# Optimization experiments

Measured on AMD Instinct MI355X. Metric: run time of the kernel, lower is better.

The kernel has to match this reference:

```python
import jax, jax.numpy as jnp
import numpy as np
import math

HIDDEN = 1024
HEADS = 16
HEAD_DIM = HIDDEN // HEADS


def setup_inputs() -> dict:
    key = jax.random.key(0)
    ks = jax.random.split(key, 7)
    B, S = 2, 2048
    scale = 1.0 / math.sqrt(HIDDEN)
    return {
        "x": jax.random.normal(ks[0], (B, S, HIDDEN), dtype=jnp.float32),
        "Wq": jax.random.normal(ks[1], (HIDDEN, HIDDEN), dtype=jnp.float32) * scale,
        "Wk": jax.random.normal(ks[2], (HIDDEN, HIDDEN), dtype=jnp.float32) * scale,
        "Wv": jax.random.normal(ks[3], (HIDDEN, HIDDEN), dtype=jnp.float32) * scale,
        "Wo": jax.random.normal(ks[4], (HIDDEN, HIDDEN), dtype=jnp.float32) * scale,
        "quantum_phase": jax.random.normal(ks[5], (HEADS, HEAD_DIM), dtype=jnp.float32),
        "quantum_amplitude": jnp.ones((HEADS, HEAD_DIM), dtype=jnp.float32),
    }


def reference(x, Wq, Wk, Wv, Wo, quantum_phase, quantum_amplitude):
    B, S, d = x.shape
    H, D = HEADS, HEAD_DIM

    # per-head/per-channel quantum modulation: real(x*exp(i*phase)) == x*cos(phase)
    mod = (jnp.cos(quantum_phase) * quantum_amplitude)[None, :, None, :]  # [1,H,1,D]

    def proj(W):
        return (x @ W).reshape(B, S, H, D).transpose(0, 2, 1, 3)  # [B,H,S,D]

    q = proj(Wq) * mod
    k = proj(Wk) * mod
    v = proj(Wv) * mod

    scores = jnp.einsum("bhid,bhjd->bhij", q, k) / math.sqrt(D)  # [B,H,S,S]

    # quantum interference: scores[i,j] *= cos(2*pi*(i-j)/S)
    idx = jnp.arange(S, dtype=jnp.float32)
    cos_mat = jnp.cos(2.0 * math.pi * (idx[:, None] - idx[None, :]) / S)  # [S,S]
    scores = scores * cos_mat

    w = jax.nn.softmax(scores, axis=-1)
    # superposition of attention weights with key-rolled copy
    w = (w + jnp.roll(w, 1, axis=-1)) / math.sqrt(2.0)

    out = jnp.einsum("bhij,bhjd->bhid", w, v)  # [B,H,S,D]
    out = out.transpose(0, 2, 1, 3).reshape(B, S, d)
    return out @ Wo
```

## Files before the change

kernel.cpp:

```cpp
#include <hip/hip_runtime.h>
#include <hip/hip_bf16.h>
#include <math.h>

#define HIDDEN 1024
#define HEADS  16
#define HDIM   64
#define BATCH  2
#define SEQ    2048
#define ROWS   (BATCH*SEQ)
#define BH     (BATCH*HEADS)

typedef __attribute__((ext_vector_type(8))) short  short8;
typedef __attribute__((ext_vector_type(8))) __bf16 bf16x8;
typedef __attribute__((ext_vector_type(4))) float  f32x4;

static __device__ __forceinline__ unsigned short f2bf(float f) {
    unsigned int u = __builtin_bit_cast(unsigned int, f);
    u += 0x7FFFu + ((u >> 16) & 1u);
    return (unsigned short)(u >> 16);
}
static __device__ __forceinline__ float bf2f(unsigned short h) {
    unsigned int u = ((unsigned int)h) << 16;
    return __builtin_bit_cast(float, u);
}
static __device__ __forceinline__ f32x4 mfma16(short8 a, short8 b, f32x4 c) {
    return __builtin_amdgcn_mfma_f32_16x16x32_bf16(
        __builtin_bit_cast(bf16x8, a), __builtin_bit_cast(bf16x8, b), c, 0, 0, 0);
}
static __device__ __forceinline__ void gl_lds16(const unsigned short* g, unsigned short* l) {
    __builtin_amdgcn_global_load_lds(
        (const __attribute__((address_space(1))) unsigned int*)g,
        (__attribute__((address_space(3))) unsigned int*)l, 16, 0, 0);
}

__global__ void convert_x_kernel(const float* __restrict__ x, unsigned short* __restrict__ xb,
                                 const float* __restrict__ qp, const float* __restrict__ qa,
                                 float* __restrict__ mod, float* __restrict__ mod2,
                                 float* __restrict__ posc, float* __restrict__ poss) {
    int i = (blockIdx.x * 256 + threadIdx.x) * 4;
    float4 v = *(const float4*)(x + i);
    ushort4 o;
    o.x = f2bf(v.x); o.y = f2bf(v.y); o.z = f2bf(v.z); o.w = f2bf(v.w);
    *(ushort4*)(xb + i) = o;
    if (blockIdx.x < 8) {
        int k = blockIdx.x * 256 + threadIdx.x;
        if (k < HIDDEN) {
            float m = cosf(qp[k]) * qa[k];
            mod[k] = m;
            mod2[k] = m * m * 0.18033688011112042f;
        }
        if (k < SEQ) {
            float ang = (float)k * (6.283185307179586f / (float)SEQ);
            posc[k] = cosf(ang);
            poss[k] = sinf(ang);
        }
    }
}

__global__ __launch_bounds__(256) void transpose_w_kernel(
    const float* __restrict__ w0, const float* __restrict__ w1,
    const float* __restrict__ w2, const float* __restrict__ w3,
    unsigned short* __restrict__ wt) {
    __shared__ unsigned short tile[64][72];
    const float* src = (blockIdx.z == 0) ? w0 : (blockIdx.z == 1) ? w1 : (blockIdx.z == 2) ? w2 : w3;
    unsigned short* dst = wt + (size_t)blockIdx.z * HIDDEN * HIDDEN;
    int n0 = blockIdx.x * 64, k0 = blockIdx.y * 64;
    int t = threadIdx.x;
    int cg = t & 15, r0 = t >> 4;
#pragma unroll
    for (int rr = 0; rr < 4; rr++) {
        int kl = r0 + rr * 16;
        float4 v = *(const float4*)(src + (size_t)(k0 + kl) * HIDDEN + n0 + cg * 4);
        tile[cg*4+0][kl] = f2bf(v.x);
        tile[cg*4+1][kl] = f2bf(v.y);
        tile[cg*4+2][kl] = f2bf(v.z);
        tile[cg*4+3][kl] = f2bf(v.w);
    }
    __syncthreads();
#pragma unroll
    for (int rr = 0; rr < 4; rr++) {
        int nl = r0 + rr * 16;
        ushort4 o;
        o.x = tile[nl][cg*4+0]; o.y = tile[nl][cg*4+1];
        o.z = tile[nl][cg*4+2]; o.w = tile[nl][cg*4+3];
        *(ushort4*)(dst + (size_t)(n0 + nl) * HIDDEN + k0 + cg * 4) = o;
    }
}

__global__ __launch_bounds__(256) void gemm_kernel(
    const unsigned short* __restrict__ A, const unsigned short* __restrict__ WtBase,
    unsigned short* __restrict__ CBase, float* __restrict__ Out, int mode0) {
    __shared__ unsigned short Alds[128 * 64];
    __shared__ unsigned short Blds[128 * 64];
    const int mode = mode0 + blockIdx.z;
    const unsigned short* Bt = WtBase + (size_t)mode * HIDDEN * HIDDEN;
    unsigned short* Cout = CBase + (size_t)mode * ROWS * HIDDEN;
    const int m0 = blockIdx.x * 128, n0 = blockIdx.y * 128;
    const int tid = threadIdx.x;
    const int wave = tid >> 6, lane = tid & 63, quad = lane >> 4, l15 = lane & 15;
    const int wr = wave >> 1, wc = wave & 1;
    const int srow = lane >> 3;
    const int schunk = (lane & 7) ^ (srow & 7);

    f32x4 acc[4][4];
    const f32x4 z4 = {0.f, 0.f, 0.f, 0.f};
#pragma unroll
    for (int i = 0; i < 4; i++)
#pragma unroll
        for (int j = 0; j < 4; j++) acc[i][j] = z4;

    for (int k0 = 0; k0 < HIDDEN; k0 += 64) {
#pragma unroll
        for (int p = 0; p < 4; p++) {
            int rbase = p * 32 + wave * 8;
            gl_lds16(A  + (size_t)(m0 + rbase + srow) * HIDDEN + k0 + schunk * 8,
                     &Alds[rbase * 64]);
            gl_lds16(Bt + (size_t)(n0 + rbase + srow) * HIDDEN + k0 + schunk * 8,
                     &Blds[rbase * 64]);
        }
        __syncthreads();
        short8 aF[4][2], bF[4][2];
#pragma unroll
        for (int h = 0; h < 2; h++) {
#pragma unroll
            for (int i = 0; i < 4; i++) {
                int row = wr * 64 + i * 16 + l15;
                aF[i][h] = *(const short8*)(&Alds[row * 64 + ((h * 4 + quad) ^ (l15 & 7)) * 8]);
            }
#pragma unroll
            for (int j = 0; j < 4; j++) {
                int row = wc * 64 + j * 16 + l15;
                bF[j][h] = *(const short8*)(&Blds[row * 64 + ((h * 4 + quad) ^ (l15 & 7)) * 8]);
            }
        }
#pragma unroll
        for (int h = 0; h < 2; h++)
#pragma unroll
            for (int i = 0; i < 4; i++)
#pragma unroll
                for (int j = 0; j < 4; j++)
                    acc[i][j] = mfma16(aF[i][h], bF[j][h], acc[i][j]);
        __syncthreads();
    }

#pragma unroll
    for (int i = 0; i < 4; i++) {
        int mbase = m0 + wr * 64 + i * 16 + quad * 4;
#pragma unroll
        for (int j = 0; j < 4; j++) {
            int n = n0 + wc * 64 + j * 16 + l15;
#pragma unroll
            for (int r = 0; r < 4; r++) {
                float val = acc[i][j][r];
                int mm = mbase + r;
                if (mode == 3) Out[(size_t)mm * HIDDEN + n] = val;
                else           Cout[(size_t)mm * HIDDEN + n] = f2bf(val);
            }
        }
    }
}

__global__ __launch_bounds__(256) void vmod_shift(const unsigned short* __restrict__ Cv,
                                                  unsigned short* __restrict__ Vpt,
                                                  const float* __restrict__ mod) {
    __shared__ unsigned short lds[65][72];
    int bh = blockIdx.x, b = bh >> 4, h = bh & 15;
    int s0 = blockIdx.y * 64;
    int t = threadIdx.x;
    int cg = t & 15, r0 = t >> 4;
    const float4 m4 = *(const float4*)(mod + h * 64 + cg * 4);
#pragma unroll
    for (int rr = 0; rr < 4; rr++) {
        int row = r0 + rr * 16;
        ushort4 v = *(const ushort4*)(Cv + ((size_t)(b * SEQ + s0 + row)) * HIDDEN + h * 64 + cg * 4);
        lds[row][cg*4+0] = f2bf(bf2f(v.x) * m4.x);
        lds[row][cg*4+1] = f2bf(bf2f(v.y) * m4.y);
        lds[row][cg*4+2] = f2bf(bf2f(v.z) * m4.z);
        lds[row][cg*4+3] = f2bf(bf2f(v.w) * m4.w);
    }
    if (t < 16) {
        int srow = (s0 + 64) & (SEQ - 1);
        const float4 mm4 = *(const float4*)(mod + h * 64 + t * 4);
        ushort4 v = *(const ushort4*)(Cv + ((size_t)(b * SEQ + srow)) * HIDDEN + h * 64 + t * 4);
        lds[64][t*4+0] = f2bf(bf2f(v.x) * mm4.x);
        lds[64][t*4+1] = f2bf(bf2f(v.y) * mm4.y);
        lds[64][t*4+2] = f2bf(bf2f(v.z) * mm4.z);
        lds[64][t*4+3] = f2bf(bf2f(v.w) * mm4.w);
    }
    __syncthreads();
    int d = t & 63, sb = (t >> 6) * 16;
    unsigned short outv[16];
#pragma unroll
    for (int k = 0; k < 16; k++) {
        float a = bf2f(lds[sb + k][d]), bb = bf2f(lds[sb + k + 1][d]);
        outv[k] = f2bf((a + bb) * 0.7071067811865476f);
    }
    unsigned short* dst = Vpt + ((size_t)bh * 64 + d) * SEQ + s0 + sb;
#pragma unroll
    for (int k = 0; k < 16; k += 4) {
        ushort4 o; o.x = outv[k]; o.y = outv[k+1]; o.z = outv[k+2]; o.w = outv[k+3];
        *(ushort4*)(dst + k) = o;
    }
}

#define KT 64
#define PSTR 76
__global__ __launch_bounds__(256) void attn_kernel(const unsigned short* __restrict__ Cq,
                                                   const unsigned short* __restrict__ Ck,
                                                   const unsigned short* __restrict__ Vpt,
                                                   unsigned short* __restrict__ Ob,
                                                   const float* __restrict__ mod2,
                                                   const float* __restrict__ posc,
                                                   const float* __restrict__ poss) {
    __shared__ unsigned short Klds[2][KT * 64];
    __shared__ unsigned short Vtlds[2][64 * 64];
    __shared__ unsigned short Plds[4 * 32 * PSTR];
    const int bh = blockIdx.x;
    const int b = bh >> 4, h = bh & 15;
    const int tid = threadIdx.x, wave = tid >> 6, lane = tid & 63;
    const int quad = lane >> 4, l15 = lane & 15;
    const int q0 = blockIdx.y * 128 + wave * 32;

    short8 qf[2][2];
#pragma unroll
    for (int g = 0; g < 2; g++) {
        int ss = q0 + g * 16 + l15;
        const unsigned short* crow = Cq + ((size_t)(b * SEQ + ss)) * HIDDEN + h * 64;
#pragma unroll
        for (int kk = 0; kk < 2; kk++) {
            int bd = kk * 32 + quad * 8;
            short8 u = *(const short8*)(crow + bd);
            short8 q;
#pragma unroll
            for (int e = 0; e < 8; e++)
                q[e] = (short)f2bf(bf2f((unsigned short)u[e]) * mod2[h * 64 + bd + e]);
            qf[g][kk] = q;
        }
    }
    float ci[2][4], si[2][4];
#pragma unroll
    for (int g = 0; g < 2; g++)
#pragma unroll
        for (int r = 0; r < 4; r++) {
            int ss = q0 + g * 16 + quad * 4 + r;
            ci[g][r] = posc[ss];
            si[g][r] = poss[ss];
        }

    const f32x4 z4 = {0.f, 0.f, 0.f, 0.f};
    f32x4 acc[2][4];
#pragma unroll
    for (int g = 0; g < 2; g++)
#pragma unroll
        for (int dt = 0; dt < 4; dt++) acc[g][dt] = z4;
    float lsum[2][4];
#pragma unroll
    for (int g = 0; g < 2; g++)
#pragma unroll
        for (int r = 0; r < 4; r++) lsum[g][r] = 0.f;

    unsigned short* pw = &Plds[wave * 32 * PSTR];

    const unsigned short* Kbh = Ck  + ((size_t)b * SEQ) * HIDDEN + h * 64;
    const unsigned short* Vbh = Vpt + (size_t)bh * 64 * SEQ;

    auto stage = [&](int j, int buf) {
#pragma unroll
        for (int p = 0; p < 2; p++) {
            int rb = p * 32 + wave * 8;
            int r  = rb + (lane >> 3);
            int c  = (lane & 7) ^ (r & 7);
            gl_lds16(Kbh + (size_t)(j + r) * HIDDEN + c * 8, &Klds[buf][rb * 64]);
        }
#pragma unroll
        for (int p = 0; p < 2; p++) {
            int rb = p * 32 + wave * 8;
            int r  = rb + (lane >> 3);
            int c  = (lane & 7) ^ (r & 7);
            gl_lds16(Vbh + (size_t)r * SEQ + j + c * 8, &Vtlds[buf][rb * 64]);
        }
    };

    stage(0, 0);
    for (int it = 0; it < SEQ / KT; it++) {
        const int j0 = it * KT;
        __syncthreads();
        if (it + 1 < SEQ / KT) stage((it + 1) * KT, (it + 1) & 1);
        const int buf = it & 1;

#pragma unroll
        for (int t2 = 0; t2 < 4; t2++) {
            float cj = posc[j0 + t2 * 16 + l15];
            float sj = poss[j0 + t2 * 16 + l15];
            f32x4 sc[2] = {z4, z4};
#pragma unroll
            for (int kk = 0; kk < 2; kk++) {
                int ch = (kk * 4 + quad) ^ (l15 & 7);
                short8 kf = *(const short8*)(&Klds[buf][(t2 * 16 + l15) * 64 + ch * 8]);
#pragma unroll
                for (int g = 0; g < 2; g++)
                    sc[g] = mfma16(qf[g][kk], kf, sc[g]);
            }
#pragma unroll
            for (int g = 0; g < 2; g++) {
#pragma unroll
                for (int r = 0; r < 4; r++) {
                    float w = ci[g][r] * cj + si[g][r] * sj;
                    float p = __builtin_amdgcn_exp2f(sc[g][r] * w);
                    unsigned short pt = (unsigned short)(__builtin_bit_cast(unsigned int, p) >> 16);
                    lsum[g][r] += bf2f(pt);
                    pw[(g * 16 + quad * 4 + r) * PSTR + t2 * 16 + l15] = pt;
                }
            }
        }

#pragma unroll
        for (int pt = 0; pt < 2; pt++) {
            short8 pa0 = *(const short8*)(&pw[(l15) * PSTR + pt * 32 + quad * 8]);
            short8 pa1 = *(const short8*)(&pw[(16 + l15) * PSTR + pt * 32 + quad * 8]);
#pragma unroll
            for (int dt = 0; dt < 4; dt++) {
                int ch = (pt * 4 + quad) ^ (l15 & 7);
                short8 vb = *(const short8*)(&Vtlds[buf][(dt * 16 + l15) * 64 + ch * 8]);
                acc[0][dt] = mfma16(pa0, vb, acc[0][dt]);
                acc[1][dt] = mfma16(pa1, vb, acc[1][dt]);
            }
        }
    }

#pragma unroll
    for (int g = 0; g < 2; g++) {
        float rinv[4];
#pragma unroll
        for (int r = 0; r < 4; r++) {
            float rs = lsum[g][r];
#pragma unroll
            for (int off = 1; off < 16; off <<= 1) rs += __shfl_xor(rs, off);
            rinv[r] = 1.0f / rs;
        }
#pragma unroll
        for (int dt = 0; dt < 4; dt++) {
#pragma unroll
            for (int r = 0; r < 4; r++) {
                int q = q0 + g * 16 + quad * 4 + r;
                int d = dt * 16 + l15;
                Ob[((size_t)(b * SEQ + q)) * HIDDEN + h * 64 + d] = f2bf(acc[g][dt][r] * rinv[r]);
            }
        }
    }
}

extern "C" void kernel_launch(void* const* d_in, const int* in_sizes, int n_in,
                              void* d_out, int out_size, void* d_ws, size_t ws_size,
                              hipStream_t stream) {
    const float* x  = (const float*)d_in[0];
    const float* Wq = (const float*)d_in[1];
    const float* Wk = (const float*)d_in[2];
    const float* Wv = (const float*)d_in[3];
    const float* Wo = (const float*)d_in[4];
    const float* qp = (const float*)d_in[5];
    const float* qa = (const float*)d_in[6];
    char* ws = (char*)d_ws;

    unsigned short* Xb  = (unsigned short*)(ws);
    unsigned short* Wt  = (unsigned short*)(ws + (size_t)( 8 << 20));
    unsigned short* Cq  = (unsigned short*)(ws + (size_t)(16 << 20));
    unsigned short* Ck  = (unsigned short*)(ws + (size_t)(24 << 20));
    unsigned short* Cv  = (unsigned short*)(ws + (size_t)(32 << 20));
    unsigned short* Vpt = (unsigned short*)(ws + (size_t)(40 << 20));
    float* mod  = (float*)(ws + (size_t)(48 << 20));
    float* mod2 = mod + 1024;
    float* posc = mod2 + 1024;
    float* poss = posc + 2048;
    float* out  = (float*)d_out;

    convert_x_kernel<<<4096, 256, 0, stream>>>(x, Xb, qp, qa, mod, mod2, posc, poss);
    transpose_w_kernel<<<dim3(16, 16, 4), 256, 0, stream>>>(Wq, Wk, Wv, Wo, Wt);
    gemm_kernel<<<dim3(32, 8, 3), 256, 0, stream>>>(Xb, Wt, Cq, out, 0);
    vmod_shift<<<dim3(32, 32), 256, 0, stream>>>(Cv, Vpt, mod);
    attn_kernel<<<dim3(32, 16), 256, 0, stream>>>(Cq, Ck, Vpt, Xb , mod2, posc, poss);
    gemm_kernel<<<dim3(32, 8, 1), 256, 0, stream>>>(Xb, Wt, Cq, out, 3);
}
```

Baseline: 254.7 us.

## Split attention over key halves with fp32 partials and a combine kernel

Attention now runs with a grid z dimension of 2, each block processing half of the key sequence and writing unnormalized fp32 numerators and row sums to workspace. A new combine kernel adds the two partials, normalizes, and writes bf16 output for the final projection. This doubles the number of attention blocks to improve GPU occupancy, at the cost of extra fp32 global traffic and one more launch. Position cos/sin values are also prefetched into registers one tile ahead.

```diff
diff --git a/kernel.cpp b/kernel.cpp
--- a/kernel.cpp
+++ b/kernel.cpp
@@ -208,7 +208,8 @@
 __global__ __launch_bounds__(256) void attn_kernel(const unsigned short* __restrict__ Cq,
                                                    const unsigned short* __restrict__ Ck,
                                                    const unsigned short* __restrict__ Vpt,
-                                                   unsigned short* __restrict__ Ob,
+                                                   float* __restrict__ Onum,
+                                                   float* __restrict__ Lsum,
                                                    const float* __restrict__ mod2,
                                                    const float* __restrict__ posc,
                                                    const float* __restrict__ poss) {
@@ -217,6 +218,8 @@
     __shared__ unsigned short Plds[4 * 32 * PSTR];
     const int bh = blockIdx.x;
     const int b = bh >> 4, h = bh & 15;
+    const int ks = blockIdx.z;
+    const int j0base = ks * (SEQ / 2);
     const int tid = threadIdx.x, wave = tid >> 6, lane = tid & 63;
     const int quad = lane >> 4, l15 = lane & 15;
     const int q0 = blockIdx.y * 128 + wave * 32;
@@ -281,17 +284,31 @@
         }
     };
 
-    stage(0, 0);
-    for (int it = 0; it < SEQ / KT; it++) {
-        const int j0 = it * KT;
+    float cjc[4], sjc[4];
+#pragma unroll
+    for (int t2 = 0; t2 < 4; t2++) {
+        int jj = j0base + t2 * 16 + l15;
+        cjc[t2] = posc[jj]; sjc[t2] = poss[jj];
+    }
+
+    stage(j0base, 0);
+    const int NIT = (SEQ / 2) / KT;
+    for (int it = 0; it < NIT; it++) {
         __syncthreads();
-        if (it + 1 < SEQ / KT) stage((it + 1) * KT, (it + 1) & 1);
+        float cjn[4], sjn[4];
+        if (it + 1 < NIT) {
+            stage(j0base + (it + 1) * KT, (it + 1) & 1);
+#pragma unroll
+            for (int t2 = 0; t2 < 4; t2++) {
+                int jj = j0base + (it + 1) * KT + t2 * 16 + l15;
+                cjn[t2] = posc[jj]; sjn[t2] = poss[jj];
+            }
+        }
         const int buf = it & 1;
 
 #pragma unroll
         for (int t2 = 0; t2 < 4; t2++) {
-            float cj = posc[j0 + t2 * 16 + l15];
-            float sj = poss[j0 + t2 * 16 + l15];
+            float cj = cjc[t2], sj = sjc[t2];
             f32x4 sc[2] = {z4, z4};
 #pragma unroll
             for (int kk = 0; kk < 2; kk++) {
@@ -326,17 +343,25 @@
                 acc[1][dt] = mfma16(pa1, vb, acc[1][dt]);
             }
         }
-    }
-
+#pragma unroll
+        for (int t2 = 0; t2 < 4; t2++) { cjc[t2] = cjn[t2]; sjc[t2] = sjn[t2]; }
+    }
+
+    float* On = Onum + (size_t)ks * ROWS * HIDDEN;
 #pragma unroll
     for (int g = 0; g < 2; g++) {
-        float rinv[4];
+        float rs4[4];
 #pragma unroll
         for (int r = 0; r < 4; r++) {
             float rs = lsum[g][r];
 #pragma unroll
             for (int off = 1; off < 16; off <<= 1) rs += __shfl_xor(rs, off);
-            rinv[r] = 1.0f / rs;
+            rs4[r] = rs;
+        }
+        if (l15 == 0) {
+#pragma unroll
+            for (int r = 0; r < 4; r++)
+                Lsum[((size_t)ks * BH + bh) * SEQ + q0 + g * 16 + quad * 4 + r] = rs4[r];
         }
 #pragma unroll
         for (int dt = 0; dt < 4; dt++) {
@@ -344,10 +369,30 @@
             for (int r = 0; r < 4; r++) {
                 int q = q0 + g * 16 + quad * 4 + r;
                 int d = dt * 16 + l15;
-                Ob[((size_t)(b * SEQ + q)) * HIDDEN + h * 64 + d] = f2bf(acc[g][dt][r] * rinv[r]);
-            }
-        }
-    }
+                On[((size_t)(b * SEQ + q)) * HIDDEN + h * 64 + d] = acc[g][dt][r];
+            }
+        }
+    }
+}
+
+__global__ __launch_bounds__(256) void combine_kernel(const float* __restrict__ Onum,
+                                                      const float* __restrict__ Lsum,
+                                                      unsigned short* __restrict__ Ob) {
+    int row = blockIdx.x;
+    int col = threadIdx.x * 4;
+    int h = col >> 6;
+    int ql = row & (SEQ - 1);
+    int bh = (row >> 11) * HEADS + h;
+    float den = Lsum[(size_t)bh * SEQ + ql] + Lsum[((size_t)BH + bh) * SEQ + ql];
+    float rinv = 1.0f / den;
+    float4 n0 = *(const float4*)(Onum + (size_t)row * HIDDEN + col);
+    float4 n1 = *(const float4*)(Onum + (size_t)ROWS * HIDDEN + (size_t)row * HIDDEN + col);
+    ushort4 o;
+    o.x = f2bf((n0.x + n1.x) * rinv);
+    o.y = f2bf((n0.y + n1.y) * rinv);
+    o.z = f2bf((n0.z + n1.z) * rinv);
+    o.w = f2bf((n0.w + n1.w) * rinv);
+    *(ushort4*)(Ob + (size_t)row * HIDDEN + col) = o;
 }
 
 extern "C" void kernel_launch(void* const* d_in, const int* in_sizes, int n_in,
@@ -362,13 +407,15 @@
     const float* qa = (const float*)d_in[6];
     char* ws = (char*)d_ws;
 
-    unsigned short* Xb  = (unsigned short*)(ws);
-    unsigned short* Wt  = (unsigned short*)(ws + (size_t)( 8 << 20));
-    unsigned short* Cq  = (unsigned short*)(ws + (size_t)(16 << 20));
-    unsigned short* Ck  = (unsigned short*)(ws + (size_t)(24 << 20));
-    unsigned short* Cv  = (unsigned short*)(ws + (size_t)(32 << 20));
-    unsigned short* Vpt = (unsigned short*)(ws + (size_t)(40 << 20));
-    float* mod  = (float*)(ws + (size_t)(48 << 20));
+    unsigned short* Xb   = (unsigned short*)(ws);
+    unsigned short* Wt   = (unsigned short*)(ws + (size_t)( 8 << 20));
+    unsigned short* Cq   = (unsigned short*)(ws + (size_t)(16 << 20));
+    unsigned short* Ck   = (unsigned short*)(ws + (size_t)(24 << 20));
+    unsigned short* Cv   = (unsigned short*)(ws + (size_t)(32 << 20));
+    unsigned short* Vpt  = (unsigned short*)(ws + (size_t)(40 << 20));
+    float* Onum = (float*)(ws + (size_t)(48 << 20));
+    float* Lsum = (float*)(ws + (size_t)(80 << 20));
+    float* mod  = (float*)(ws + (size_t)(81 << 20));
     float* mod2 = mod + 1024;
     float* posc = mod2 + 1024;
     float* poss = posc + 2048;
@@ -378,6 +425,7 @@
     transpose_w_kernel<<<dim3(16, 16, 4), 256, 0, stream>>>(Wq, Wk, Wv, Wo, Wt);
     gemm_kernel<<<dim3(32, 8, 3), 256, 0, stream>>>(Xb, Wt, Cq, out, 0);
     vmod_shift<<<dim3(32, 32), 256, 0, stream>>>(Cv, Vpt, mod);
-    attn_kernel<<<dim3(32, 16), 256, 0, stream>>>(Cq, Ck, Vpt, Xb , mod2, posc, poss);
+    attn_kernel<<<dim3(32, 16, 2), 256, 0, stream>>>(Cq, Ck, Vpt, Onum, Lsum, mod2, posc, poss);
+    combine_kernel<<<ROWS, 256, 0, stream>>>(Onum, Lsum, Xb );
     gemm_kernel<<<dim3(32, 8, 1), 256, 0, stream>>>(Xb, Wt, Cq, out, 3);
 }
```

Result: slower. 261.0 us (+2.4%).
